# Performance work log

Hardware: AMD Instinct MI355X
Metric: run time of the kernel (lower is better)

Reference implementation:

```python
import jax, jax.numpy as jnp
import numpy as np

N_NODES = 100000
N_EDGES = 3200000
NFEAT = 512
NHID = 256
KEEP_PROB = 0.5  # dropout p = 0.5


def setup_inputs() -> dict:
    key = jax.random.key(0)
    ks = jax.random.split(key, 9)
    x = jax.random.normal(ks[0], (N_NODES, NFEAT), dtype=jnp.float32)
    W1 = jax.random.normal(ks[1], (NFEAT, NHID), dtype=jnp.float32) * (1.0 / np.sqrt(NFEAT))
    b1 = jax.random.normal(ks[2], (NHID,), dtype=jnp.float32) * 0.01
    W2 = jax.random.normal(ks[3], (NHID, NHID), dtype=jnp.float32) * (1.0 / np.sqrt(NHID))
    b2 = jax.random.normal(ks[4], (NHID,), dtype=jnp.float32) * 0.01
    edge_row = jnp.sort(jax.random.randint(ks[5], (N_EDGES,), 0, N_NODES, dtype=jnp.int64))
    edge_col = jax.random.randint(ks[6], (N_EDGES,), 0, N_NODES, dtype=jnp.int64)
    edge_weight = jax.random.uniform(ks[7], (N_EDGES,), dtype=jnp.float32)
    drop_u = jax.random.uniform(ks[8], (N_NODES, NHID), dtype=jnp.float32)
    return {"x": x, "W1": W1, "b1": b1, "W2": W2, "b2": b2,
            "edge_row": edge_row, "edge_col": edge_col,
            "edge_weight": edge_weight, "drop_u": drop_u}


def reference(x, W1, b1, W2, b2, edge_row, edge_col, edge_weight, drop_u):
    n = x.shape[0]

    def spmm(h):
        # out[i] = sum_j adj[i, j] * h[j]  (COO gather + segment-sum)
        msg = h[edge_col] * edge_weight[:, None]  # [E, d]
        return jax.ops.segment_sum(msg, edge_row, num_segments=n)

    # layer 1: relu(spmm(adj, x @ W1) + b1)
    h = jax.nn.relu(spmm(x @ W1) + b1)
    # deterministic dropout (training=True, p=0.5): keep where u < keep_prob, scale by 1/keep
    mask = (drop_u < KEEP_PROB).astype(h.dtype)
    h = h * mask / KEEP_PROB
    # layer 2: relu(spmm(adj, h @ W2) + b2)
    h = jax.nn.relu(spmm(h @ W2) + b2)
    return jax.nn.log_softmax(h, axis=1)
```

## Files before the change

### kernel.cpp

```cpp
#include <hip/hip_runtime.h>
#include <stdint.h>

#define N_NODES 100000
#define N_EDGES 3200000
#define NFEAT 512
#define NHID 256
#define MPAD 100096

typedef __attribute__((ext_vector_type(8))) short bf16x8_t;
typedef __attribute__((ext_vector_type(8))) unsigned short u16x8_t;
typedef __attribute__((ext_vector_type(4))) float f32x4_t;
typedef __attribute__((ext_vector_type(2))) float f32x2_t;
typedef __attribute__((ext_vector_type(4))) unsigned int u32x4_t;

#define RFL(x) __builtin_amdgcn_readfirstlane(x)

__device__ inline unsigned short f2bf(float f) {
  union { float f; uint32_t u; } x; x.f = f;
  uint32_t r = x.u + 0x7fffu + ((x.u >> 16) & 1u);
  return (unsigned short)(r >> 16);
}
__device__ inline float b2f(unsigned short u) {
  union { uint32_t u; float f; } x; x.u = ((uint32_t)u) << 16;
  return x.f;
}
__device__ inline float asf(uint32_t u) {
  union { uint32_t u; float f; } x; x.u = u;
  return x.f;
}

__global__ void prep_k(const float* __restrict__ W1, const float* __restrict__ W2,
                       unsigned short* __restrict__ W1T, unsigned short* __restrict__ W2T) {
  int i = blockIdx.x * 256 + threadIdx.x;
  if (i < NFEAT * NHID) {
    int k = i >> 8, n = i & 255;
    W1T[n * NFEAT + k] = f2bf(W1[i]);
  } else {
    int j = i - NFEAT * NHID;
    int k = j >> 8, n = j & 255;
    W2T[n * NHID + k] = f2bf(W2[j]);
  }
}

__global__ void rowptr_k(const int* __restrict__ erow, int* __restrict__ rowptr) {
  int r = blockIdx.x * 256 + threadIdx.x;
  if (r > N_NODES) return;
  int lo = 0, hi = N_EDGES;
  while (lo < hi) {
    int mid = (lo + hi) >> 1;
    if (erow[mid] < r) lo = mid + 1; else hi = mid;
  }
  rowptr[r] = lo;
}

template <bool A_FP32>
__global__ __launch_bounds__(512) void gemm_bt2(const void* __restrict__ Ap,
                                                const unsigned short* __restrict__ BT,
                                                unsigned short* __restrict__ C,
                                                int K, int Mreal) {
  __shared__ __align__(16) unsigned short As[128 * 64];
  __shared__ __align__(16) unsigned short Bs[256 * 64];
  const int tid = threadIdx.x;
  const int lane = tid & 63, wid = tid >> 6;
  const int wm = wid >> 2, wn = wid & 3;
  const int m0 = blockIdx.x * 128;
  const int lrow = lane & 15, lhi = lane >> 4;

  f32x4_t acc[4][4] = {};

  const int nt = K >> 6;
  for (int t = 0; t < nt; ++t) {
    __syncthreads();
    if constexpr (A_FP32) {
      const float* A = (const float*)Ap;
      const int rr = tid >> 4;
      const int kq = (tid & 15) << 2;
#pragma unroll
      for (int round = 0; round < 4; ++round) {
        int row = rr + (round << 5);
        int grow = m0 + row; grow = grow < Mreal ? grow : Mreal - 1;
        const f32x4_t v = __builtin_nontemporal_load(
            (const f32x4_t*)(A + (size_t)grow * K + (t << 6) + kq));
        ushort4 b4;
        b4.x = f2bf(v.x); b4.y = f2bf(v.y); b4.z = f2bf(v.z); b4.w = f2bf(v.w);
        *(ushort4*)&As[(row << 6) + (kq ^ ((row & 7) << 3))] = b4;
      }
    } else {
      const unsigned short* A = (const unsigned short*)Ap;
      const int Lrow = tid >> 3;
      const int Lc = (tid & 7) << 4;
#pragma unroll
      for (int round = 0; round < 2; ++round) {
        int row = Lrow + (round << 6);
        int srcc = Lc ^ ((row & 7) << 4);
        const char* g = (const char*)(A + (size_t)(m0 + row) * K + (t << 6)) + srcc;
        __builtin_amdgcn_global_load_lds(
            (const __attribute__((address_space(1))) void*)g,
            (__attribute__((address_space(3))) void*)((char*)As + tid * 16 + (round << 13)),
            16, 0, 0);
      }
    }
    {
      const int Lrow = tid >> 3;
      const int Lc = (tid & 7) << 4;
#pragma unroll
      for (int round = 0; round < 4; ++round) {
        int row = Lrow + (round << 6);
        int srcc = Lc ^ ((row & 7) << 4);
        const char* g = (const char*)(BT + (size_t)row * K + (t << 6)) + srcc;
        __builtin_amdgcn_global_load_lds(
            (const __attribute__((address_space(1))) void*)g,
            (__attribute__((address_space(3))) void*)((char*)Bs + tid * 16 + (round << 13)),
            16, 0, 0);
      }
    }
    asm volatile("s_waitcnt vmcnt(0)" ::: "memory");
    __syncthreads();

#pragma unroll
    for (int ks = 0; ks < 2; ++ks) {
      bf16x8_t af[4], bfr[4];
      const int cu = (ks << 5) + (lhi << 3);
#pragma unroll
      for (int mf = 0; mf < 4; ++mf) {
        int row = (wm << 6) + (mf << 4) + lrow;
        af[mf] = *(const bf16x8_t*)&As[(row << 6) + (cu ^ ((row & 7) << 3))];
      }
#pragma unroll
      for (int nf = 0; nf < 4; ++nf) {
        int row = (wn << 6) + (nf << 4) + lrow;
        bfr[nf] = *(const bf16x8_t*)&Bs[(row << 6) + (cu ^ ((row & 7) << 3))];
      }
#pragma unroll
      for (int mf = 0; mf < 4; ++mf)
#pragma unroll
        for (int nf = 0; nf < 4; ++nf)
          acc[mf][nf] = __builtin_amdgcn_mfma_f32_16x16x32_bf16(af[mf], bfr[nf], acc[mf][nf], 0, 0, 0);
    }
  }

#pragma unroll
  for (int mf = 0; mf < 4; ++mf)
#pragma unroll
    for (int nf = 0; nf < 4; ++nf)
#pragma unroll
      for (int j = 0; j < 4; ++j) {
        int gm = m0 + (wm << 6) + (mf << 4) + (lhi << 2) + j;
        int gn = (wn << 6) + (nf << 4) + lrow;
        C[(size_t)gm * 256 + gn] = f2bf(acc[mf][nf][j]);
      }
}

#define LOADP4(V, W, EB)                                             \
  _Pragma("unroll")                                                  \
  for (int q = 0; q < 4; ++q) {                                      \
    uint32_t ce = (uint32_t)RFL(ecol[(EB) + 2 * q]);                 \
    uint32_t co = (uint32_t)RFL(ecol[(EB) + 2 * q + 1]);             \
    uint32_t ue = RFL(__float_as_uint(ew[(EB) + 2 * q]));            \
    uint32_t uo = RFL(__float_as_uint(ew[(EB) + 2 * q + 1]));        \
    uint32_t cv = lo ? ce : co;                                      \
    W[q] = __uint_as_float(lo ? ue : uo);                            \
    V[q] = *(const u32x4_t*)(Xb + (((size_t)cv << 9) + c16));        \
  }
#define CONSP4(V, W)                                                 \
  _Pragma("unroll")                                                  \
  for (int q = 0; q < 4; ++q) {                                      \
    f32x2_t w2_; w2_.x = W[q]; w2_.y = W[q];                         \
    f32x2_t v0_, v1_, v2_, v3_;                                      \
    v0_.x = asf(V[q].x << 16); v0_.y = asf(V[q].x & 0xffff0000u);    \
    v1_.x = asf(V[q].y << 16); v1_.y = asf(V[q].y & 0xffff0000u);    \
    v2_.x = asf(V[q].z << 16); v2_.y = asf(V[q].z & 0xffff0000u);    \
    v3_.x = asf(V[q].w << 16); v3_.y = asf(V[q].w & 0xffff0000u);    \
    fa0 += v0_ * w2_; fa1 += v1_ * w2_;                              \
    fa2 += v2_ * w2_; fa3 += v3_ * w2_;                              \
  }

#define GATHER_ROW()                                                 \
  f32x2_t fa0 = {}, fa1 = {}, fa2 = {}, fa3 = {};                    \
  {                                                                  \
    u32x4_t va[4], vb[4]; float wa[4], wb[4];                        \
    if (e + 8 <= e1) {                                               \
      LOADP4(va, wa, e);                                             \
      for (; e + 24 <= e1; e += 16) {                                \
        LOADP4(vb, wb, e + 8);                                       \
        CONSP4(va, wa);                                              \
        LOADP4(va, wa, e + 16);                                      \
        CONSP4(vb, wb);                                              \
      }                                                              \
      if (e + 16 <= e1) {                                            \
        LOADP4(vb, wb, e + 8);                                       \
        CONSP4(va, wa);                                              \
        CONSP4(vb, wb);                                              \
        e += 16;                                                     \
      } else { CONSP4(va, wa); e += 8; }                             \
    }                                                                \
    for (; e + 2 <= e1; e += 2) {              \
      uint32_t ce_ = (uint32_t)RFL(ecol[e]);                         \
      uint32_t co_ = (uint32_t)RFL(ecol[e + 1]);                     \
      uint32_t ue_ = RFL(__float_as_uint(ew[e]));                    \
      uint32_t uo_ = RFL(__float_as_uint(ew[e + 1]));                \
      u32x4_t vr[1]; float wr[1];                                    \
      wr[0] = __uint_as_float(lo ? ue_ : uo_);                       \
      vr[0] = *(const u32x4_t*)(Xb + (((size_t)(lo ? ce_ : co_) << 9) + c16)); \
      _Pragma("unroll")                                              \
      for (int q = 0; q < 1; ++q) {                                  \
        f32x2_t w2_; w2_.x = wr[q]; w2_.y = wr[q];                   \
        f32x2_t v0_, v1_, v2_, v3_;                                  \
        v0_.x = asf(vr[q].x << 16); v0_.y = asf(vr[q].x & 0xffff0000u); \
        v1_.x = asf(vr[q].y << 16); v1_.y = asf(vr[q].y & 0xffff0000u); \
        v2_.x = asf(vr[q].z << 16); v2_.y = asf(vr[q].z & 0xffff0000u); \
        v3_.x = asf(vr[q].w << 16); v3_.y = asf(vr[q].w & 0xffff0000u); \
        fa0 += v0_ * w2_; fa1 += v1_ * w2_;                          \
        fa2 += v2_ * w2_; fa3 += v3_ * w2_;                          \
      }                                                              \
    }                                                                \
    if (e < e1) {          \
      uint32_t c_ = (uint32_t)RFL(ecol[e]);                          \
      float w_ = __uint_as_float(RFL(__float_as_uint(ew[e])));       \
      u32x4_t v_ = *(const u32x4_t*)(Xb + (((size_t)c_ << 9) + c16)); \
      float wv_ = lo ? w_ : 0.0f;                                    \
      f32x2_t w2_; w2_.x = wv_; w2_.y = wv_;                         \
      f32x2_t v0_, v1_, v2_, v3_;                                    \
      v0_.x = asf(v_.x << 16); v0_.y = asf(v_.x & 0xffff0000u);      \
      v1_.x = asf(v_.y << 16); v1_.y = asf(v_.y & 0xffff0000u);      \
      v2_.x = asf(v_.z << 16); v2_.y = asf(v_.z & 0xffff0000u);      \
      v3_.x = asf(v_.w << 16); v3_.y = asf(v_.w & 0xffff0000u);      \
      fa0 += v0_ * w2_; fa1 += v1_ * w2_;                            \
      fa2 += v2_ * w2_; fa3 += v3_ * w2_;                            \
    }                                                                \
  }                                                                  \
  float f[8];                                                        \
  f[0] = fa0.x; f[1] = fa0.y; f[2] = fa1.x; f[3] = fa1.y;            \
  f[4] = fa2.x; f[5] = fa2.y; f[6] = fa3.x; f[7] = fa3.y;            \
  _Pragma("unroll")                                                  \
  for (int j = 0; j < 8; ++j) f[j] += __shfl_xor(f[j], 32);

__global__ __launch_bounds__(256) void spmm1_k(const unsigned short* __restrict__ XW1,
                                               const int* __restrict__ rowptr,
                                               const int* __restrict__ ecol,
                                               const float* __restrict__ ew,
                                               const float* __restrict__ b1,
                                               const float* __restrict__ du,
                                               unsigned short* __restrict__ H) {
  const int lane = threadIdx.x & 63, wid = threadIdx.x >> 6;
  const int r = blockIdx.x * 4 + wid;
  const bool lo = lane < 32;
  const int g = lane & 31;
  const uint32_t c16 = (uint32_t)g << 4;
  if (r >= N_NODES) {
    if (lo) {
      u16x8_t z;
#pragma unroll
      for (int j = 0; j < 8; ++j) z[j] = 0;
      *(u16x8_t*)&H[(size_t)r * 256 + (g << 3)] = z;
    }
    return;
  }
  const char* Xb = (const char*)XW1;
  int e  = RFL(rowptr[r]);
  const int e1 = RFL(rowptr[r + 1]);
  GATHER_ROW();
  if (lo) {
    const int g8 = g << 3;
    float bv[8], uu[8];
    *(f32x4_t*)&bv[0] = *(const f32x4_t*)&b1[g8];
    *(f32x4_t*)&bv[4] = *(const f32x4_t*)&b1[g8 + 4];
    *(f32x4_t*)&uu[0] = __builtin_nontemporal_load((const f32x4_t*)&du[(size_t)r * 256 + g8]);
    *(f32x4_t*)&uu[4] = __builtin_nontemporal_load((const f32x4_t*)&du[(size_t)r * 256 + g8 + 4]);
    u16x8_t o;
#pragma unroll
    for (int j = 0; j < 8; ++j) {
      float h = fmaxf(f[j] + bv[j], 0.f) * (uu[j] < 0.5f ? 2.f : 0.f);
      o[j] = f2bf(h);
    }
    *(u16x8_t*)&H[(size_t)r * 256 + g8] = o;
  }
}

__global__ __launch_bounds__(256) void spmm2_k(const unsigned short* __restrict__ HW2,
                                               const int* __restrict__ rowptr,
                                               const int* __restrict__ ecol,
                                               const float* __restrict__ ew,
                                               const float* __restrict__ b2,
                                               float* __restrict__ out) {
  const int lane = threadIdx.x & 63, wid = threadIdx.x >> 6;
  const int r = blockIdx.x * 4 + wid;
  if (r >= N_NODES) return;
  const bool lo = lane < 32;
  const int g = lane & 31;
  const uint32_t c16 = (uint32_t)g << 4;
  const char* Xb = (const char*)HW2;
  int e  = RFL(rowptr[r]);
  const int e1 = RFL(rowptr[r + 1]);
  GATHER_ROW();
  const int g8 = g << 3;
  float bv[8];
  *(f32x4_t*)&bv[0] = *(const f32x4_t*)&b2[g8];
  *(f32x4_t*)&bv[4] = *(const f32x4_t*)&b2[g8 + 4];
  float v[8];
#pragma unroll
  for (int j = 0; j < 8; ++j) v[j] = fmaxf(f[j] + bv[j], 0.f);
  float m = v[0];
#pragma unroll
  for (int j = 1; j < 8; ++j) m = fmaxf(m, v[j]);
#pragma unroll
  for (int off = 16; off > 0; off >>= 1) m = fmaxf(m, __shfl_xor(m, off));
  float s = 0.f;
#pragma unroll
  for (int j = 0; j < 8; ++j) s += expf(v[j] - m);
#pragma unroll
  for (int off = 16; off > 0; off >>= 1) s += __shfl_xor(s, off);
  const float ls = m + logf(s);
  if (lo) {
    f32x4_t o0, o1;
    o0.x = v[0] - ls; o0.y = v[1] - ls; o0.z = v[2] - ls; o0.w = v[3] - ls;
    o1.x = v[4] - ls; o1.y = v[5] - ls; o1.z = v[6] - ls; o1.w = v[7] - ls;
    __builtin_nontemporal_store(o0, (f32x4_t*)&out[(size_t)r * 256 + g8]);
    __builtin_nontemporal_store(o1, (f32x4_t*)&out[(size_t)r * 256 + g8 + 4]);
  }
}

extern "C" void kernel_launch(void* const* d_in, const int* in_sizes, int n_in,
                              void* d_out, int out_size, void* d_ws, size_t ws_size,
                              hipStream_t stream) {
  const float* x  = (const float*)d_in[0];
  const float* W1 = (const float*)d_in[1];
  const float* b1 = (const float*)d_in[2];
  const float* W2 = (const float*)d_in[3];
  const float* b2 = (const float*)d_in[4];
  const int* erow = (const int*)d_in[5];
  const int* ecol = (const int*)d_in[6];
  const float* ew = (const float*)d_in[7];
  const float* du = (const float*)d_in[8];
  float* out = (float*)d_out;

  char* ws = (char*)d_ws;
  unsigned short* W1T = (unsigned short*)ws;
  unsigned short* W2T = (unsigned short*)(ws + 262144);
  int* rowptr = (int*)(ws + 262144 + 131072);
  unsigned short* XW1 = (unsigned short*)(ws + 262144 + 131072 + 401408);
  unsigned short* H = (unsigned short*)(ws + 262144 + 131072 + 401408 + 51249152);

  prep_k<<<768, 256, 0, stream>>>(W1, W2, W1T, W2T);
  rowptr_k<<<392, 256, 0, stream>>>(erow, rowptr);
  gemm_bt2<true><<<782, 512, 0, stream>>>((const void*)x, W1T, XW1, NFEAT, N_NODES);
  spmm1_k<<<MPAD / 4, 256, 0, stream>>>(XW1, rowptr, ecol, ew, b1, du, H);
  gemm_bt2<false><<<782, 512, 0, stream>>>((const void*)H, W2T, XW1, NHID, MPAD);
  spmm2_k<<<N_NODES / 4, 256, 0, stream>>>(XW1, rowptr, ecol, ew, b2, out);
}
```

Measured before the change: 550.5 us.

## Bucket-sort each row's edges by column block to improve gather locality

Adds a per-row kernel that reorders each row's edges (column index and weight) into 13 buckets of column>>13, using wave ballots, and writes them to new workspace arrays. Both SpMM kernels then read the reordered edges, so concurrently running rows gather feature rows from nearby column ranges and should hit L2/MALL more often. The cost is an extra pass over the edge arrays every call, plus added workspace. It only runs when the workspace is large enough. A small cleanup flattens the single-iteration tail loop in the SpMM macro.

```diff
diff --git a/kernel.cpp b/kernel.cpp
--- a/kernel.cpp
+++ b/kernel.cpp
@@ -51,6 +51,52 @@
     if (erow[mid] < r) lo = mid + 1; else hi = mid;
   }
   rowptr[r] = lo;
+}
+
+__global__ __launch_bounds__(256) void esort_k(const int* __restrict__ rowptr,
+                                               const int* __restrict__ ecol,
+                                               const float* __restrict__ ew,
+                                               int* __restrict__ ecol2,
+                                               float* __restrict__ ew2) {
+  const int r = blockIdx.x * 4 + (threadIdx.x >> 6);
+  if (r >= N_NODES) return;
+  const int lane = threadIdx.x & 63;
+  const int e0 = rowptr[r], e1 = rowptr[r + 1];
+  const int deg = e1 - e0;
+  const unsigned long long below = (1ull << lane) - 1ull;
+  if (deg <= 64) {
+    const int idx = e0 + lane;
+    const bool valid = idx < e1;
+    const int c = valid ? ecol[idx] : 0x7fffffff;
+    const float w = valid ? ew[idx] : 0.f;
+    const int b = c >> 13;
+    int off = 0, myrank = 0;
+#pragma unroll 1
+    for (int bb = 0; bb < 13; ++bb) {
+      unsigned long long mask = __ballot(valid && b == bb);
+      if (valid && b == bb) myrank = off + __popcll(mask & below);
+      off += __popcll(mask);
+    }
+    if (valid) { ecol2[e0 + myrank] = c; ew2[e0 + myrank] = w; }
+  } else {
+    int off = 0;
+#pragma unroll 1
+    for (int bb = 0; bb < 13; ++bb) {
+      for (int base = e0; base < e1; base += 64) {
+        const int idx = base + lane;
+        const bool valid = idx < e1;
+        const int c = valid ? ecol[idx] : 0x7fffffff;
+        const int b = c >> 13;
+        unsigned long long mask = __ballot(valid && b == bb);
+        if (valid && b == bb) {
+          int rank = off + __popcll(mask & below);
+          ecol2[e0 + rank] = c;
+          ew2[e0 + rank] = ew[idx];
+        }
+        off += __popcll(mask);
+      }
+    }
+  }
 }
 
 template <bool A_FP32>
@@ -194,27 +240,24 @@
         e += 16;                                                     \
       } else { CONSP4(va, wa); e += 8; }                             \
     }                                                                \
-    for (; e + 2 <= e1; e += 2) {              \
+    for (; e + 2 <= e1; e += 2) {                                    \
       uint32_t ce_ = (uint32_t)RFL(ecol[e]);                         \
       uint32_t co_ = (uint32_t)RFL(ecol[e + 1]);                     \
       uint32_t ue_ = RFL(__float_as_uint(ew[e]));                    \
       uint32_t uo_ = RFL(__float_as_uint(ew[e + 1]));                \
-      u32x4_t vr[1]; float wr[1];                                    \
-      wr[0] = __uint_as_float(lo ? ue_ : uo_);                       \
-      vr[0] = *(const u32x4_t*)(Xb + (((size_t)(lo ? ce_ : co_) << 9) + c16)); \
-      _Pragma("unroll")                                              \
-      for (int q = 0; q < 1; ++q) {                                  \
-        f32x2_t w2_; w2_.x = wr[q]; w2_.y = wr[q];                   \
-        f32x2_t v0_, v1_, v2_, v3_;                                  \
-        v0_.x = asf(vr[q].x << 16); v0_.y = asf(vr[q].x & 0xffff0000u); \
-        v1_.x = asf(vr[q].y << 16); v1_.y = asf(vr[q].y & 0xffff0000u); \
-        v2_.x = asf(vr[q].z << 16); v2_.y = asf(vr[q].z & 0xffff0000u); \
-        v3_.x = asf(vr[q].w << 16); v3_.y = asf(vr[q].w & 0xffff0000u); \
-        fa0 += v0_ * w2_; fa1 += v1_ * w2_;                          \
-        fa2 += v2_ * w2_; fa3 += v3_ * w2_;                          \
-      }                                                              \
+      u32x4_t vr; float wr;                                          \
+      wr = __uint_as_float(lo ? ue_ : uo_);                          \
+      vr = *(const u32x4_t*)(Xb + (((size_t)(lo ? ce_ : co_) << 9) + c16)); \
+      f32x2_t w2_; w2_.x = wr; w2_.y = wr;                           \
+      f32x2_t v0_, v1_, v2_, v3_;                                    \
+      v0_.x = asf(vr.x << 16); v0_.y = asf(vr.x & 0xffff0000u);      \
+      v1_.x = asf(vr.y << 16); v1_.y = asf(vr.y & 0xffff0000u);      \
+      v2_.x = asf(vr.z << 16); v2_.y = asf(vr.z & 0xffff0000u);      \
+      v3_.x = asf(vr.w << 16); v3_.y = asf(vr.w & 0xffff0000u);      \
+      fa0 += v0_ * w2_; fa1 += v1_ * w2_;                            \
+      fa2 += v2_ * w2_; fa3 += v3_ * w2_;                            \
     }                                                                \
-    if (e < e1) {          \
+    if (e < e1) {                                                    \
       uint32_t c_ = (uint32_t)RFL(ecol[e]);                          \
       float w_ = __uint_as_float(RFL(__float_as_uint(ew[e])));       \
       u32x4_t v_ = *(const u32x4_t*)(Xb + (((size_t)c_ << 9) + c16)); \
@@ -338,13 +381,25 @@
   unsigned short* W1T = (unsigned short*)ws;
   unsigned short* W2T = (unsigned short*)(ws + 262144);
   int* rowptr = (int*)(ws + 262144 + 131072);
-  unsigned short* XW1 = (unsigned short*)(ws + 262144 + 131072 + 401408);
-  unsigned short* H = (unsigned short*)(ws + 262144 + 131072 + 401408 + 51249152);
+  unsigned short* XW1 = (unsigned short*)(ws + 794624);
+  unsigned short* H = (unsigned short*)(ws + 794624 + 51249152);
+  int* ecol2 = (int*)(ws + 794624 + 2 * 51249152);
+  float* ew2 = (float*)(ws + 794624 + 2 * 51249152 + 12800000);
+  const size_t NEED = 794624 + 2ull * 51249152 + 2ull * 12800000;
 
   prep_k<<<768, 256, 0, stream>>>(W1, W2, W1T, W2T);
   rowptr_k<<<392, 256, 0, stream>>>(erow, rowptr);
+
+  const int* gecol = ecol;
+  const float* gew = ew;
+  if (ws_size >= NEED) {
+    esort_k<<<25000, 256, 0, stream>>>(rowptr, ecol, ew, ecol2, ew2);
+    gecol = ecol2;
+    gew = ew2;
+  }
+
   gemm_bt2<true><<<782, 512, 0, stream>>>((const void*)x, W1T, XW1, NFEAT, N_NODES);
-  spmm1_k<<<MPAD / 4, 256, 0, stream>>>(XW1, rowptr, ecol, ew, b1, du, H);
+  spmm1_k<<<MPAD / 4, 256, 0, stream>>>(XW1, rowptr, gecol, gew, b1, du, H);
   gemm_bt2<false><<<782, 512, 0, stream>>>((const void*)H, W2T, XW1, NHID, MPAD);
-  spmm2_k<<<N_NODES / 4, 256, 0, stream>>>(XW1, rowptr, ecol, ew, b2, out);
-}
+  spmm2_k<<<N_NODES / 4, 256, 0, stream>>>(XW1, rowptr, gecol, gew, b2, out);
+}
```

After: 576.9 us. 1.05x slower.
